# Optimization experiments

Measured on AMD Instinct MI355X. Metric: run time of the kernel, lower is better.

The kernel has to match this reference:

```python
import jax, jax.numpy as jnp
import numpy as np
from jax import lax

N, D = 16384, 512
E_SPEC, E_SHARED = 8, 2


def setup_inputs() -> dict:
    key = jax.random.key(0)
    ks = jax.random.split(key, 7)
    return {
        "x": jax.random.normal(ks[0], (N, D), dtype=jnp.float32),
        "spec_router_logits": jax.random.normal(ks[1], (N, E_SPEC), dtype=jnp.float32),
        "shared_router_logits": jax.random.normal(ks[2], (N, E_SHARED), dtype=jnp.float32),
        "spec_W": jax.random.normal(ks[3], (E_SPEC, D, D), dtype=jnp.float32) * 0.02,
        "spec_b": jax.random.normal(ks[4], (E_SPEC, D), dtype=jnp.float32) * 0.02,
        "shared_W": jax.random.normal(ks[5], (E_SHARED, D, D), dtype=jnp.float32) * 0.02,
        "shared_b": jax.random.normal(ks[6], (E_SHARED, D), dtype=jnp.float32) * 0.02,
        "top_k": 2,
    }


def reference(x, spec_router_logits, shared_router_logits, spec_W, spec_b, shared_W, shared_b, top_k):
    n, e_spec = spec_router_logits.shape
    # --- specific experts: top-k routing with renormalized weights ---
    spec_probs = jax.nn.softmax(spec_router_logits, axis=1)          # [N, E_spec]
    topk_w, topk_idx = lax.top_k(spec_probs, top_k)                  # [N, K]
    topk_w = topk_w / (jnp.sum(topk_w, axis=1, keepdims=True) + 1e-6)
    # dense per-token per-expert weight matrix (zero for unselected), matching
    # the original dense mask-accumulate loop
    weights = jnp.zeros((n, e_spec), dtype=spec_probs.dtype)
    weights = weights.at[jnp.arange(n)[:, None], topk_idx].add(topk_w)  # [N, E_spec]
    # dense eval of all specific experts (Linear d->d), then weighted combine
    spec_outs = jnp.einsum('nd,edf->enf', x, spec_W) + spec_b[:, None, :]  # [E,N,D]
    spec_out = jnp.einsum('ne,enf->nf', weights, spec_outs)                # [N,D]
    # --- shared experts: soft combine over softmax probs ---
    shared_probs = jax.nn.softmax(shared_router_logits, axis=1)           # [N, E_shared]
    shared_outs = jnp.einsum('nd,edf->enf', x, shared_W) + shared_b[:, None, :]
    shared_out = jnp.einsum('ne,enf->nf', shared_probs, shared_outs)
    return spec_out + shared_out
```

## Files before the change

kernel.cpp:

```cpp
#include <hip/hip_runtime.h>
#include <stdint.h>

typedef unsigned short ushort_t;
typedef __attribute__((ext_vector_type(8))) short short8;
typedef __attribute__((ext_vector_type(4))) float f32x4;
typedef __attribute__((ext_vector_type(4))) unsigned int u32x4;

#define TOK  16384
#define DIM  512
#define NEXP 10

__device__ __forceinline__ unsigned short f2bf(float f) {
  union { float f; uint32_t u; } v; v.f = f;
  uint32_t u = v.u;
  uint32_t r = (u + 0x7fffu + ((u >> 16) & 1u)) >> 16;
  return (unsigned short)r;
}
__device__ __forceinline__ float bflo_to_f(uint32_t u) {
  union { uint32_t u; float f; } v; v.u = u << 16; return v.f;
}
__device__ __forceinline__ float bfhi_to_f(uint32_t u) {
  union { uint32_t u; float f; } v; v.u = u & 0xffff0000u; return v.f;
}

__global__ void k_router(const float* __restrict__ sl, const float* __restrict__ shl,
                         float* __restrict__ c) {
  int n = blockIdx.x * 256 + threadIdx.x;
  if (n >= TOK) return;
  float l[8];
  float m = -1e30f;
#pragma unroll
  for (int i = 0; i < 8; ++i) { l[i] = sl[n*8 + i]; m = fmaxf(m, l[i]); }
  float s = 0.f;
#pragma unroll
  for (int i = 0; i < 8; ++i) { l[i] = expf(l[i] - m); s += l[i]; }
  float inv = 1.f / s;
#pragma unroll
  for (int i = 0; i < 8; ++i) l[i] *= inv;
  int i1 = 0; float v1 = l[0];
#pragma unroll
  for (int i = 1; i < 8; ++i) if (l[i] > v1) { v1 = l[i]; i1 = i; }
  int i2 = -1; float v2 = -1.f;
#pragma unroll
  for (int i = 0; i < 8; ++i) if (i != i1 && l[i] > v2) { v2 = l[i]; i2 = i; }
  float rs = 1.f / (v1 + v2 + 1e-6f);
  float w1 = v1 * rs, w2 = v2 * rs;
#pragma unroll
  for (int i = 0; i < 8; ++i) {
    float oi = (i == i1) ? w1 : ((i == i2) ? w2 : 0.f);
    c[n*NEXP + i] = oi;
  }
  float s0 = shl[n*2], s1 = shl[n*2 + 1];
  float mm = fmaxf(s0, s1);
  float e0 = expf(s0 - mm), e1 = expf(s1 - mm);
  float si = 1.f / (e0 + e1);
  c[n*NEXP + 8] = e0 * si;
  c[n*NEXP + 9] = e1 * si;
}

__global__ void k_cvtx(const float* __restrict__ x, ushort_t* __restrict__ xb) {
  int i = (blockIdx.x * 256 + threadIdx.x) * 8;
  f32x4 v0 = *(const f32x4*)(x + i);
  f32x4 v1 = *(const f32x4*)(x + i + 4);
  u32x4 o;
  o[0] = (uint32_t)f2bf(v0[0]) | ((uint32_t)f2bf(v0[1]) << 16);
  o[1] = (uint32_t)f2bf(v0[2]) | ((uint32_t)f2bf(v0[3]) << 16);
  o[2] = (uint32_t)f2bf(v1[0]) | ((uint32_t)f2bf(v1[1]) << 16);
  o[3] = (uint32_t)f2bf(v1[2]) | ((uint32_t)f2bf(v1[3]) << 16);
  *(u32x4*)(xb + i) = o;
}

__global__ void k_trw(const float* __restrict__ wspec, const float* __restrict__ wsh,
                      ushort_t* __restrict__ wt) {
  __shared__ float t[32][33];
  int e = blockIdx.z;
  const float* src = (e < 8) ? (wspec + e * DIM * DIM) : (wsh + (e - 8) * DIM * DIM);
  int tx = threadIdx.x, ty = threadIdx.y;
  int d = blockIdx.y * 32 + ty, f = blockIdx.x * 32 + tx;
  t[ty][tx] = src[d * DIM + f];
  __syncthreads();
  int fo = blockIdx.x * 32 + ty, dd = blockIdx.y * 32 + tx;
  wt[(size_t)e * DIM * DIM + fo * DIM + dd] = f2bf(t[tx][ty]);
}

__global__ __launch_bounds__(256, 2)
void k_moe(const ushort_t* __restrict__ xb, const ushort_t* __restrict__ wt,
           const float* __restrict__ cws, const float* __restrict__ bspec,
           const float* __restrict__ bsh, float* __restrict__ out) {
  __shared__ ushort_t aB[2][128 * 64];
  __shared__ ushort_t bB[2][128 * 64];
  __shared__ float cT[NEXP * 128];
  __shared__ float bT[NEXP * 128];

  const int tid  = threadIdx.x;
  const int lane = tid & 63;
  const int w    = tid >> 6;
  const int wr   = w >> 1, wc = w & 1;
  const int bid  = blockIdx.x;
  const int trow = (bid & 127) << 7;
  const int tcol = (bid >> 7) << 7;

  for (int i = tid; i < NEXP * 128; i += 256) {
    int r = i / NEXP, e = i - r * NEXP;
    cT[e * 128 + r] = cws[(trow + r) * NEXP + e];
  }
  for (int i = tid; i < NEXP * 128; i += 256) {
    int e = i >> 7, col = i & 127;
    bT[i] = (e < 8) ? bspec[e * DIM + tcol + col] : bsh[(e - 8) * DIM + tcol + col];
  }

  int goff[4];
  const int pb = (w << 12) + (lane << 4);
#pragma unroll
  for (int i = 0; i < 4; ++i) {
    int p   = pb + (i << 10);
    int row = p >> 7;
    int kb  = (p & 127) ^ ((row & 7) << 4);
    goff[i] = row * DIM + (kb >> 1);
  }
  const ushort_t* aSrc     = xb + trow * DIM;
  const ushort_t* bSrcBase = wt + tcol * DIM;

  auto stageA = [&](int ks, int buf) {
    const ushort_t* s = aSrc + (ks << 6);
#pragma unroll
    for (int i = 0; i < 4; ++i)
      __builtin_amdgcn_global_load_lds(
          (const __attribute__((address_space(1))) void*)(s + goff[i]),
          (__attribute__((address_space(3))) void*)((char*)(&aB[buf][0]) + (w << 12) + (i << 10)),
          16, 0, 0);
  };
  auto stageB = [&](int ks, int e, int buf) {
    const ushort_t* s = bSrcBase + (e << 18) + (ks << 6);
#pragma unroll
    for (int i = 0; i < 4; ++i)
      __builtin_amdgcn_global_load_lds(
          (const __attribute__((address_space(1))) void*)(s + goff[i]),
          (__attribute__((address_space(3))) void*)((char*)(&bB[buf][0]) + (w << 12) + (i << 10)),
          16, 0, 0);
  };

  f32x4 acc[4][4];
#pragma unroll
  for (int a = 0; a < 4; ++a)
#pragma unroll
    for (int b = 0; b < 4; ++b) acc[a][b] = (f32x4){0.f, 0.f, 0.f, 0.f};

  stageA(0, 0);
  stageB(0, 0, 0);

  float a32[4][2][8];

  for (int ks = 0; ks < 8; ++ks) {
    for (int e = 0; e < NEXP; ++e) {
      __syncthreads();
      if (e < 9)        stageB(ks, e + 1, (e + 1) & 1);
      else if (ks < 7)  stageB(ks + 1, 0, 0);
      if (e == 8 && ks < 7) stageA(ks + 1, (ks + 1) & 1);

      if (e == 0) {
        const char* ab = (const char*)(&aB[ks & 1][0]);
#pragma unroll
        for (int rb = 0; rb < 4; ++rb) {
          int row = wr * 64 + rb * 16 + (lane & 15);
#pragma unroll
          for (int ksl = 0; ksl < 2; ++ksl) {
            int kb = ((ksl << 6) + ((lane >> 4) << 4)) ^ ((row & 7) << 4);
            u32x4 v = *(const u32x4*)(ab + row * 128 + kb);
#pragma unroll
            for (int j = 0; j < 4; ++j) {
              a32[rb][ksl][2 * j]     = bflo_to_f(v[j]);
              a32[rb][ksl][2 * j + 1] = bfhi_to_f(v[j]);
            }
          }
        }
      }

      float ce[4];
#pragma unroll
      for (int rb = 0; rb < 4; ++rb)
        ce[rb] = cT[(e << 7) + wr * 64 + rb * 16 + (lane & 15)];

      const char* bb = (const char*)(&bB[e & 1][0]);
      u32x4 bf4[2][4];
#pragma unroll
      for (int ksl = 0; ksl < 2; ++ksl)
#pragma unroll
        for (int cb = 0; cb < 4; ++cb) {
          int col = wc * 64 + cb * 16 + (lane & 15);
          int kb  = ((ksl << 6) + ((lane >> 4) << 4)) ^ ((col & 7) << 4);
          bf4[ksl][cb] = *(const u32x4*)(bb + col * 128 + kb);
        }

#pragma unroll
      for (int ksl = 0; ksl < 2; ++ksl) {
#pragma unroll
        for (int rb = 0; rb < 4; ++rb) {
          u32x4 q;
#pragma unroll
          for (int j = 0; j < 4; ++j) {
            float lo = a32[rb][ksl][2 * j]     * ce[rb];
            float hi = a32[rb][ksl][2 * j + 1] * ce[rb];
            uint32_t r;
            asm("v_cvt_pk_bf16_f32 %0, %1, %2" : "=v"(r) : "v"(lo), "v"(hi));
            q[j] = r;
          }
          short8 a8 = __builtin_bit_cast(short8, q);
#pragma unroll
          for (int cb = 0; cb < 4; ++cb) {
            short8 b8 = __builtin_bit_cast(short8, bf4[ksl][cb]);
            acc[rb][cb] = __builtin_amdgcn_mfma_f32_16x16x32_bf16(a8, b8, acc[rb][cb], 0, 0, 0);
          }
        }
      }
    }
  }

#pragma unroll
  for (int rb = 0; rb < 4; ++rb) {
    int rloc = wr * 64 + rb * 16 + ((lane >> 4) << 2);
    f32x4 cv[NEXP];
#pragma unroll
    for (int e2 = 0; e2 < NEXP; ++e2)
      cv[e2] = *(const f32x4*)&cT[e2 * 128 + rloc];
#pragma unroll
    for (int cb = 0; cb < 4; ++cb) {
      int cloc = wc * 64 + cb * 16 + (lane & 15);
      f32x4 a = acc[rb][cb];
#pragma unroll
      for (int e2 = 0; e2 < NEXP; ++e2) {
        float bv = bT[e2 * 128 + cloc];
        a[0] += cv[e2][0] * bv;
        a[1] += cv[e2][1] * bv;
        a[2] += cv[e2][2] * bv;
        a[3] += cv[e2][3] * bv;
      }
      float* o = out + (size_t)(trow + rloc) * DIM + (tcol + cloc);
      o[0 * DIM] = a[0];
      o[1 * DIM] = a[1];
      o[2 * DIM] = a[2];
      o[3 * DIM] = a[3];
    }
  }
}

extern "C" void kernel_launch(void* const* d_in, const int* in_sizes, int n_in,
                              void* d_out, int out_size, void* d_ws, size_t ws_size,
                              hipStream_t stream) {
  (void)in_sizes; (void)n_in; (void)out_size; (void)ws_size;
  const float* x   = (const float*)d_in[0];
  const float* srl = (const float*)d_in[1];
  const float* shl = (const float*)d_in[2];
  const float* sW  = (const float*)d_in[3];
  const float* sb  = (const float*)d_in[4];
  const float* hW  = (const float*)d_in[5];
  const float* hb  = (const float*)d_in[6];
  float* out = (float*)d_out;

  float*    cws = (float*)d_ws;
  ushort_t* xb  = (ushort_t*)(cws + TOK * NEXP);
  ushort_t* wt  = xb + (size_t)TOK * DIM;

  k_router<<<TOK / 256, 256, 0, stream>>>(srl, shl, cws);
  k_cvtx<<<(TOK * DIM) / (8 * 256), 256, 0, stream>>>(x, xb);
  dim3 tb(32, 32, 1), tg(16, 16, 10);
  k_trw<<<tg, tb, 0, stream>>>(sW, hW, wt);
  k_moe<<<512, 256, 0, stream>>>(xb, wt, cws, sb, hb, out);
}
```

Before: 110.8 us.

## Group tokens by top-2 expert pair to skip unselected expert GEMMs

Replaces dense evaluation of all 10 experts per token with a routing pipeline. Tokens are bucketed by their sorted top-2 expert pair via atomic counts, a serial scan and a scatter fill. Each block then gathers 128 same-pair tokens and runs only 4 GEMMs (two chosen specific experts plus two shared). Per-expert weights are applied to fp32 accumulators instead of scaling bf16 A fragments. This cuts matrix work from 10 experts to 4 per token, at the cost of extra small launches, a single-thread scan, gathered A loads, scattered output stores and padded partial tiles.

After: 179.7 us. 1.62x slower.

```diff
diff --git a/kernel.cpp b/kernel.cpp
--- a/kernel.cpp
+++ b/kernel.cpp
@@ -8,7 +8,8 @@
 
 #define TOK  16384
 #define DIM  512
-#define NEXP 10
+#define NPAIR 64
+#define MAXROWTILES 156
 
 __device__ __forceinline__ unsigned short f2bf(float f) {
   union { float f; uint32_t u; } v; v.f = f;
@@ -16,15 +17,10 @@
   uint32_t r = (u + 0x7fffu + ((u >> 16) & 1u)) >> 16;
   return (unsigned short)r;
 }
-__device__ __forceinline__ float bflo_to_f(uint32_t u) {
-  union { uint32_t u; float f; } v; v.u = u << 16; return v.f;
-}
-__device__ __forceinline__ float bfhi_to_f(uint32_t u) {
-  union { uint32_t u; float f; } v; v.u = u & 0xffff0000u; return v.f;
-}
 
 __global__ void k_router(const float* __restrict__ sl, const float* __restrict__ shl,
-                         float* __restrict__ c) {
+                         float* __restrict__ w4, int* __restrict__ pairid,
+                         int* __restrict__ cnt) {
   int n = blockIdx.x * 256 + threadIdx.x;
   if (n >= TOK) return;
   float l[8];
@@ -45,17 +41,44 @@
   for (int i = 0; i < 8; ++i) if (i != i1 && l[i] > v2) { v2 = l[i]; i2 = i; }
   float rs = 1.f / (v1 + v2 + 1e-6f);
   float w1 = v1 * rs, w2 = v2 * rs;
-#pragma unroll
-  for (int i = 0; i < 8; ++i) {
-    float oi = (i == i1) ? w1 : ((i == i2) ? w2 : 0.f);
-    c[n*NEXP + i] = oi;
-  }
+  int pmin, pmax; float wa, wb;
+  if (i1 < i2) { pmin = i1; pmax = i2; wa = w1; wb = w2; }
+  else         { pmin = i2; pmax = i1; wa = w2; wb = w1; }
   float s0 = shl[n*2], s1 = shl[n*2 + 1];
   float mm = fmaxf(s0, s1);
   float e0 = expf(s0 - mm), e1 = expf(s1 - mm);
   float si = 1.f / (e0 + e1);
-  c[n*NEXP + 8] = e0 * si;
-  c[n*NEXP + 9] = e1 * si;
+  w4[n*4 + 0] = wa;
+  w4[n*4 + 1] = wb;
+  w4[n*4 + 2] = e0 * si;
+  w4[n*4 + 3] = e1 * si;
+  int p = pmin * 8 + pmax;
+  pairid[n] = p;
+  atomicAdd(&cnt[p], 1);
+}
+
+__global__ void k_scan(const int* __restrict__ cnt, int* __restrict__ off,
+                       int* __restrict__ cursor, int* __restrict__ ts,
+                       ushort_t* __restrict__ idx) {
+  if (blockIdx.x == 0 && threadIdx.x == 0) {
+    int a = 0, t = 0;
+    for (int p = 0; p < NPAIR; ++p) {
+      off[p] = a; cursor[p] = a; ts[p] = t;
+      a += cnt[p];
+      t += (cnt[p] + 127) >> 7;
+    }
+    ts[NPAIR] = t;
+    for (int i = 0; i < 128; ++i) idx[TOK + i] = 0;
+  }
+}
+
+__global__ void k_fill(const int* __restrict__ pairid, int* __restrict__ cursor,
+                       ushort_t* __restrict__ idx) {
+  int n = blockIdx.x * 256 + threadIdx.x;
+  if (n >= TOK) return;
+  int p = pairid[n];
+  int s = atomicAdd(&cursor[p], 1);
+  idx[s] = (ushort_t)n;
 }
 
 __global__ void k_cvtx(const float* __restrict__ x, ushort_t* __restrict__ xb) {
@@ -85,161 +108,166 @@
 
 __global__ __launch_bounds__(256, 2)
 void k_moe(const ushort_t* __restrict__ xb, const ushort_t* __restrict__ wt,
-           const float* __restrict__ cws, const float* __restrict__ bspec,
+           const float* __restrict__ w4, const ushort_t* __restrict__ idx,
+           const int* __restrict__ off, const int* __restrict__ cnt,
+           const int* __restrict__ ts, const float* __restrict__ bspec,
            const float* __restrict__ bsh, float* __restrict__ out) {
   __shared__ ushort_t aB[2][128 * 64];
   __shared__ ushort_t bB[2][128 * 64];
-  __shared__ float cT[NEXP * 128];
-  __shared__ float bT[NEXP * 128];
+  __shared__ float wLT[4 * 128];
+  __shared__ float bL[4 * 128];
+  __shared__ int   iL[128];
 
   const int tid  = threadIdx.x;
   const int lane = tid & 63;
   const int w    = tid >> 6;
   const int wr   = w >> 1, wc = w & 1;
-  const int bid  = blockIdx.x;
-  const int trow = (bid & 127) << 7;
-  const int tcol = (bid >> 7) << 7;
-
-  for (int i = tid; i < NEXP * 128; i += 256) {
-    int r = i / NEXP, e = i - r * NEXP;
-    cT[e * 128 + r] = cws[(trow + r) * NEXP + e];
-  }
-  for (int i = tid; i < NEXP * 128; i += 256) {
-    int e = i >> 7, col = i & 127;
-    bT[i] = (e < 8) ? bspec[e * DIM + tcol + col] : bsh[(e - 8) * DIM + tcol + col];
-  }
-
-  int goff[4];
+
+  int bx   = blockIdx.x;
+  int slot = (bx & 7) * 78 + (bx >> 3);
+  int r    = slot >> 2, cdx = slot & 3;
+  if (r >= ts[NPAIR]) return;
+  int p = 0;
+#pragma unroll 1
+  for (int q = 0; q < NPAIR; ++q) { if (r >= ts[q] && r < ts[q + 1]) { p = q; break; } }
+  const int tstart = r - ts[p];
+  const int base   = off[p] + (tstart << 7);
+  int cl = cnt[p] - (tstart << 7); if (cl > 128) cl = 128;
+  const int e0 = p >> 3, e1 = p & 7;
+  const int tcol = cdx << 7;
+
+  for (int i = tid; i < 128; i += 256) iL[i] = (int)idx[base + i];
+  for (int i = tid; i < 512; i += 256) {
+    int j = i >> 7, rs = i & 127;
+    wLT[i] = (rs < cl) ? w4[(int)idx[base + rs] * 4 + j] : 0.f;
+  }
+  for (int i = tid; i < 512; i += 256) {
+    int j = i >> 7, col = i & 127;
+    int e = (j == 0) ? e0 : (j == 1) ? e1 : (j == 2) ? 8 : 9;
+    bL[i] = (e < 8) ? bspec[e * DIM + tcol + col] : bsh[(e - 8) * DIM + tcol + col];
+  }
+
+  int aoff[4], boff[4];
   const int pb = (w << 12) + (lane << 4);
 #pragma unroll
   for (int i = 0; i < 4; ++i) {
-    int p   = pb + (i << 10);
-    int row = p >> 7;
-    int kb  = (p & 127) ^ ((row & 7) << 4);
-    goff[i] = row * DIM + (kb >> 1);
-  }
-  const ushort_t* aSrc     = xb + trow * DIM;
-  const ushort_t* bSrcBase = wt + tcol * DIM;
+    int pp  = pb + (i << 10);
+    int row = pp >> 7;
+    int kb  = (pp & 127) ^ ((row & 7) << 4);
+    int tok = (int)idx[base + row];
+    aoff[i] = tok * DIM + (kb >> 1);
+    boff[i] = (tcol + row) * DIM + (kb >> 1);
+  }
 
   auto stageA = [&](int ks, int buf) {
-    const ushort_t* s = aSrc + (ks << 6);
 #pragma unroll
     for (int i = 0; i < 4; ++i)
       __builtin_amdgcn_global_load_lds(
-          (const __attribute__((address_space(1))) void*)(s + goff[i]),
+          (const __attribute__((address_space(1))) void*)(xb + aoff[i] + (ks << 6)),
           (__attribute__((address_space(3))) void*)((char*)(&aB[buf][0]) + (w << 12) + (i << 10)),
           16, 0, 0);
   };
-  auto stageB = [&](int ks, int e, int buf) {
-    const ushort_t* s = bSrcBase + (e << 18) + (ks << 6);
+  auto stageB = [&](int e, int ks, int buf) {
+    const ushort_t* s = wt + ((size_t)e << 18) + (ks << 6);
 #pragma unroll
     for (int i = 0; i < 4; ++i)
       __builtin_amdgcn_global_load_lds(
-          (const __attribute__((address_space(1))) void*)(s + goff[i]),
+          (const __attribute__((address_space(1))) void*)(s + boff[i]),
           (__attribute__((address_space(3))) void*)((char*)(&bB[buf][0]) + (w << 12) + (i << 10)),
           16, 0, 0);
   };
 
-  f32x4 acc[4][4];
+  f32x4 accO[4][4];
 #pragma unroll
   for (int a = 0; a < 4; ++a)
 #pragma unroll
-    for (int b = 0; b < 4; ++b) acc[a][b] = (f32x4){0.f, 0.f, 0.f, 0.f};
+    for (int b = 0; b < 4; ++b) accO[a][b] = (f32x4){0.f, 0.f, 0.f, 0.f};
 
   stageA(0, 0);
-  stageB(0, 0, 0);
-
-  float a32[4][2][8];
-
-  for (int ks = 0; ks < 8; ++ks) {
-    for (int e = 0; e < NEXP; ++e) {
+  stageB(e0, 0, 0);
+
+#pragma unroll 1
+  for (int j = 0; j < 4; ++j) {
+    f32x4 acc[4][4];
+#pragma unroll
+    for (int a = 0; a < 4; ++a)
+#pragma unroll
+      for (int b = 0; b < 4; ++b) acc[a][b] = (f32x4){0.f, 0.f, 0.f, 0.f};
+
+#pragma unroll 1
+    for (int ks = 0; ks < 8; ++ks) {
+      int s = (j << 3) | ks;
       __syncthreads();
-      if (e < 9)        stageB(ks, e + 1, (e + 1) & 1);
-      else if (ks < 7)  stageB(ks + 1, 0, 0);
-      if (e == 8 && ks < 7) stageA(ks + 1, (ks + 1) & 1);
-
-      if (e == 0) {
-        const char* ab = (const char*)(&aB[ks & 1][0]);
-#pragma unroll
-        for (int rb = 0; rb < 4; ++rb) {
-          int row = wr * 64 + rb * 16 + (lane & 15);
-#pragma unroll
-          for (int ksl = 0; ksl < 2; ++ksl) {
-            int kb = ((ksl << 6) + ((lane >> 4) << 4)) ^ ((row & 7) << 4);
-            u32x4 v = *(const u32x4*)(ab + row * 128 + kb);
-#pragma unroll
-            for (int j = 0; j < 4; ++j) {
-              a32[rb][ksl][2 * j]     = bflo_to_f(v[j]);
-              a32[rb][ksl][2 * j + 1] = bfhi_to_f(v[j]);
-            }
-          }
+      if (s < 31) {
+        int ns = s + 1, nks = ns & 7, nj = ns >> 3, nbuf = ns & 1;
+        int ne = (nj == 0) ? e0 : (nj == 1) ? e1 : (nj == 2) ? 8 : 9;
+        stageA(nks, nbuf);
+        stageB(ne, nks, nbuf);
+      }
+      const int buf = s & 1;
+      const char* ab = (const char*)(&aB[buf][0]);
+      const char* bb = (const char*)(&bB[buf][0]);
+      u32x4 af[4][2], bf[4][2];
+#pragma unroll
+      for (int rb = 0; rb < 4; ++rb) {
+        int row = wr * 64 + rb * 16 + (lane & 15);
+#pragma unroll
+        for (int ksl = 0; ksl < 2; ++ksl) {
+          int kb = ((ksl << 6) + ((lane >> 4) << 4)) ^ ((row & 7) << 4);
+          af[rb][ksl] = *(const u32x4*)(ab + row * 128 + kb);
         }
       }
-
-      float ce[4];
-#pragma unroll
-      for (int rb = 0; rb < 4; ++rb)
-        ce[rb] = cT[(e << 7) + wr * 64 + rb * 16 + (lane & 15)];
-
-      const char* bb = (const char*)(&bB[e & 1][0]);
-      u32x4 bf4[2][4];
+#pragma unroll
+      for (int cb = 0; cb < 4; ++cb) {
+        int col = wc * 64 + cb * 16 + (lane & 15);
+#pragma unroll
+        for (int ksl = 0; ksl < 2; ++ksl) {
+          int kb = ((ksl << 6) + ((lane >> 4) << 4)) ^ ((col & 7) << 4);
+          bf[cb][ksl] = *(const u32x4*)(bb + col * 128 + kb);
+        }
+      }
 #pragma unroll
       for (int ksl = 0; ksl < 2; ++ksl)
 #pragma unroll
-        for (int cb = 0; cb < 4; ++cb) {
-          int col = wc * 64 + cb * 16 + (lane & 15);
-          int kb  = ((ksl << 6) + ((lane >> 4) << 4)) ^ ((col & 7) << 4);
-          bf4[ksl][cb] = *(const u32x4*)(bb + col * 128 + kb);
-        }
-
-#pragma unroll
-      for (int ksl = 0; ksl < 2; ++ksl) {
-#pragma unroll
         for (int rb = 0; rb < 4; ++rb) {
-          u32x4 q;
-#pragma unroll
-          for (int j = 0; j < 4; ++j) {
-            float lo = a32[rb][ksl][2 * j]     * ce[rb];
-            float hi = a32[rb][ksl][2 * j + 1] * ce[rb];
-            uint32_t r;
-            asm("v_cvt_pk_bf16_f32 %0, %1, %2" : "=v"(r) : "v"(lo), "v"(hi));
-            q[j] = r;
-          }
-          short8 a8 = __builtin_bit_cast(short8, q);
+          short8 a8 = __builtin_bit_cast(short8, af[rb][ksl]);
 #pragma unroll
           for (int cb = 0; cb < 4; ++cb) {
-            short8 b8 = __builtin_bit_cast(short8, bf4[ksl][cb]);
+            short8 b8 = __builtin_bit_cast(short8, bf[cb][ksl]);
             acc[rb][cb] = __builtin_amdgcn_mfma_f32_16x16x32_bf16(a8, b8, acc[rb][cb], 0, 0, 0);
           }
         }
-      }
+    }
+#pragma unroll
+    for (int rb = 0; rb < 4; ++rb) {
+      int rloc = wr * 64 + rb * 16 + ((lane >> 4) << 2);
+      f32x4 wv = *(const f32x4*)&wLT[(j << 7) + rloc];
+#pragma unroll
+      for (int cb = 0; cb < 4; ++cb) accO[rb][cb] += wv * acc[rb][cb];
     }
   }
 
 #pragma unroll
   for (int rb = 0; rb < 4; ++rb) {
     int rloc = wr * 64 + rb * 16 + ((lane >> 4) << 2);
-    f32x4 cv[NEXP];
-#pragma unroll
-    for (int e2 = 0; e2 < NEXP; ++e2)
-      cv[e2] = *(const f32x4*)&cT[e2 * 128 + rloc];
+    f32x4 wv[4];
+#pragma unroll
+    for (int j = 0; j < 4; ++j) wv[j] = *(const f32x4*)&wLT[(j << 7) + rloc];
+    int tok[4]; bool pr[4];
+#pragma unroll
+    for (int q = 0; q < 4; ++q) { int rs = rloc + q; pr[q] = rs < cl; tok[q] = iL[rs]; }
 #pragma unroll
     for (int cb = 0; cb < 4; ++cb) {
       int cloc = wc * 64 + cb * 16 + (lane & 15);
-      f32x4 a = acc[rb][cb];
-#pragma unroll
-      for (int e2 = 0; e2 < NEXP; ++e2) {
-        float bv = bT[e2 * 128 + cloc];
-        a[0] += cv[e2][0] * bv;
-        a[1] += cv[e2][1] * bv;
-        a[2] += cv[e2][2] * bv;
-        a[3] += cv[e2][3] * bv;
+      f32x4 v = accO[rb][cb];
+#pragma unroll
+      for (int j = 0; j < 4; ++j) {
+        float bj = bL[(j << 7) + cloc];
+        v += wv[j] * bj;
       }
-      float* o = out + (size_t)(trow + rloc) * DIM + (tcol + cloc);
-      o[0 * DIM] = a[0];
-      o[1 * DIM] = a[1];
-      o[2 * DIM] = a[2];
-      o[3 * DIM] = a[3];
+#pragma unroll
+      for (int q = 0; q < 4; ++q)
+        if (pr[q]) out[(size_t)tok[q] * DIM + tcol + cloc] = v[q];
     }
   }
 }
@@ -257,13 +285,23 @@
   const float* hb  = (const float*)d_in[6];
   float* out = (float*)d_out;
 
-  float*    cws = (float*)d_ws;
-  ushort_t* xb  = (ushort_t*)(cws + TOK * NEXP);
-  ushort_t* wt  = xb + (size_t)TOK * DIM;
-
-  k_router<<<TOK / 256, 256, 0, stream>>>(srl, shl, cws);
+  char* ws = (char*)d_ws;
+  float*    w4     = (float*)ws;                           ws += TOK * 4 * 4;
+  int*      pairid = (int*)ws;                             ws += TOK * 4;
+  ushort_t* idx    = (ushort_t*)ws;                        ws += (TOK + 128) * 2 + 256;
+  int*      cntp   = (int*)ws;                             ws += NPAIR * 4;
+  int*      offp   = (int*)ws;                             ws += NPAIR * 4;
+  int*      curp   = (int*)ws;                             ws += NPAIR * 4;
+  int*      tsp    = (int*)ws;                             ws += (NPAIR + 1) * 4 + 252;
+  ushort_t* xb     = (ushort_t*)ws;                        ws += (size_t)TOK * DIM * 2;
+  ushort_t* wt     = (ushort_t*)ws;
+
+  hipMemsetAsync(cntp, 0, NPAIR * sizeof(int), stream);
+  k_router<<<TOK / 256, 256, 0, stream>>>(srl, shl, w4, pairid, cntp);
+  k_scan<<<1, 64, 0, stream>>>(cntp, offp, curp, tsp, idx);
+  k_fill<<<TOK / 256, 256, 0, stream>>>(pairid, curp, idx);
   k_cvtx<<<(TOK * DIM) / (8 * 256), 256, 0, stream>>>(x, xb);
   dim3 tb(32, 32, 1), tg(16, 16, 10);
   k_trw<<<tg, tb, 0, stream>>>(sW, hW, wt);
-  k_moe<<<512, 256, 0, stream>>>(xb, wt, cws, sb, hb, out);
-}
+  k_moe<<<MAXROWTILES * 4, 256, 0, stream>>>(xb, wt, w4, idx, offp, cntp, tsp, sb, hb, out);
+}
```
